# Performance work log

Hardware: AMD Instinct MI355X
Metric: run time of the kernel (lower is better)

## Reference

```python
import jax, jax.numpy as jnp
import numpy as np

GRID = 128
N = GRID * GRID  # number of torus nodes, node id v = x + GRID * y
HID = 64
OUT = 1
BATCH = 64


def _neighbor_idx():
    # Replicates gen_neighbor_lists: sparse matrices are permutation gathers
    # (A x)[v] = x[neighbor(v)] on a periodic grid.
    idx = np.arange(N)
    xc = idx % GRID
    yc = idx // GRID
    up = xc + ((yc + 1) % GRID) * GRID
    down = xc + ((yc - 1) % GRID) * GRID
    left = (xc - 1) % GRID + yc * GRID
    right = (xc + 1) % GRID + yc * GRID
    return np.stack([up, down, left, right], axis=0).astype(np.int32)  # [4, N]

NBR = jnp.asarray(_neighbor_idx())


def setup_inputs() -> dict:
    key = jax.random.key(0)
    ks = jax.random.split(key, 7)
    s4, sh = 1.0 / np.sqrt(4.0), 1.0 / np.sqrt(HID)
    return {
        "x": jax.random.normal(ks[0], (BATCH, N, 2), dtype=jnp.float32),
        "H": jnp.eye(2, dtype=jnp.float32),
        "W_emb": jax.random.uniform(ks[1], (4, HID), jnp.float32, -s4, s4),
        "b_emb": jax.random.uniform(ks[2], (HID,), jnp.float32, -s4, s4),
        "W_hid": jax.random.uniform(ks[3], (HID, HID), jnp.float32, -sh, sh),
        "b_hid": jax.random.uniform(ks[4], (HID,), jnp.float32, -sh, sh),
        "W_post": jax.random.uniform(ks[5], (HID, OUT), jnp.float32, -sh, sh),
        "b_post": jax.random.uniform(ks[6], (OUT,), jnp.float32, -sh, sh),
    }


def reference(x, H, W_emb, b_emb, W_hid, b_hid, W_post, b_post):
    # Permutation-matrix sparse.mm == direct neighbor gather: [B, 4, N, 2]
    xn = x[:, NBR, :]
    # Bilinear form per direction/node: s[b,i,k] = sum_{m,n} x[b,i,m] H[m,n] xn[b,k,i,n]
    s = jnp.einsum('bim,bkin,mn->bik', x, xn, H)  # [B, N, 4]
    h = jax.nn.relu(s @ W_emb + b_emb)            # [B, N, HID]
    h = jax.nn.relu(h @ W_hid + b_hid)            # [B, N, HID]
    h = h @ W_post + b_post                       # [B, N, OUT]
    return h.sum(axis=1)                          # [B, OUT]
```

## Files before the change

kernel.cpp:

```cpp
#include <hip/hip_runtime.h>
#include <hip/hip_bf16.h>

#define GRID_D 128
#define NSITES (GRID_D * GRID_D)
#define HID 64
#define BATCH 64

#define WPB 4
#define BLOCKS 2048
#define BLOCKS_PER_BATCH (BLOCKS / BATCH)
#define WAVES_PER_BATCH (BLOCKS_PER_BATCH * WPB)
#define TILES_PER_WAVE (NSITES / (WAVES_PER_BATCH * 16))

typedef short bf16x8 __attribute__((ext_vector_type(8)));
typedef float f32x4  __attribute__((ext_vector_type(4)));

__device__ __forceinline__ unsigned short f2bf(float f) {
    return __builtin_bit_cast(unsigned short, __float2bfloat16(f));
}

__device__ __forceinline__ unsigned cvt_pk_bf16(float a, float b) {
    unsigned r;
    asm("v_cvt_pk_bf16_f32 %0, %1, %2" : "=v"(r) : "v"(a), "v"(b));
    return r;
}

union frag_u { bf16x8 v; unsigned u[4]; unsigned short us[8]; };

__global__ __launch_bounds__(256)
void gauge_mfma(const float* __restrict__ x,
                const float* __restrict__ H,
                const float* __restrict__ W_emb,
                const float* __restrict__ b_emb,
                const float* __restrict__ W_hid,
                const float* __restrict__ b_hid,
                const float* __restrict__ W_post,
                float* __restrict__ ws)
{
    const int tid   = threadIdx.x;
    const int lane  = tid & 63;
    const int widx  = tid >> 6;
    const int wgid  = blockIdx.x * WPB + widx;
    const int b     = wgid / WAVES_PER_BATCH;
    const int wslot = wgid % WAVES_PER_BATCH;

    const int  ls  = lane & 15;
    const int  kg  = lane >> 4;
    const bool kg0 = (kg == 0);

    const float h00 = H[0], h01 = H[1], h10 = H[2], h11 = H[3];

    bf16x8 bfrag[4][2];
    #pragma unroll
    for (int t = 0; t < 4; ++t) {
        #pragma unroll
        for (int s = 0; s < 2; ++s) {
            frag_u r;
            #pragma unroll
            for (int i = 0; i < 8; ++i) {
                const int khid = s * 32 + ((i & 4) << 2) + (kg << 2) + (i & 3);
                r.us[i] = f2bf(W_hid[khid * HID + t * 16 + ls]);
            }
            bfrag[t][s] = r.v;
        }
    }

    bf16x8 afe[4];
    #pragma unroll
    for (int m = 0; m < 4; ++m) {
        const int col = m * 16 + ls;
        const float w0 = W_emb[0 * HID + col];
        const float w1 = W_emb[1 * HID + col];
        const float w2 = W_emb[2 * HID + col];
        const float w3 = W_emb[3 * HID + col];
        const float bb = b_emb[col];
        frag_u r;
        r.u[0] = kg0 ? cvt_pk_bf16(w0, w1) : 0u;
        r.u[1] = kg0 ? cvt_pk_bf16(w2, w3) : 0u;
        r.u[2] = kg0 ? (unsigned)f2bf(bb) : 0u;
        r.u[3] = 0u;
        afe[m] = r.v;
    }

    float bh[4], wp[4];
    #pragma unroll
    for (int t = 0; t < 4; ++t) {
        bh[t] = b_hid[t * 16 + ls];
        wp[t] = W_post[t * 16 + ls];
    }

    const float* __restrict__ xb = x + (size_t)b * NSITES * 2;
    const int wbase = wslot * (16 * TILES_PER_WAVE);
    const unsigned sd2 = kg0 ? 0x00003F80u : 0u;
    float o = 0.0f;

    for (int tile = 0; tile < TILES_PER_WAVE; ++tile) {
        const int site = wbase + tile * 16 + ls;
        const int xc = site & (GRID_D - 1);
        const int yc = site >> 7;
        const int n0 = xc + (((yc + 1) & (GRID_D - 1)) << 7);
        const int n1 = xc + (((yc - 1) & (GRID_D - 1)) << 7);
        const int n2 = ((xc - 1) & (GRID_D - 1)) + (yc << 7);
        const int n3 = ((xc + 1) & (GRID_D - 1)) + (yc << 7);

        const float2 xi = *(const float2*)(xb + 2 * site);
        const float2 xu = *(const float2*)(xb + 2 * n0);
        const float2 xd = *(const float2*)(xb + 2 * n1);
        const float2 xl = *(const float2*)(xb + 2 * n2);
        const float2 xr = *(const float2*)(xb + 2 * n3);

        const float s0 = xi.x * fmaf(h00, xu.x, h01 * xu.y) + xi.y * fmaf(h10, xu.x, h11 * xu.y);
        const float s1 = xi.x * fmaf(h00, xd.x, h01 * xd.y) + xi.y * fmaf(h10, xd.x, h11 * xd.y);
        const float s2 = xi.x * fmaf(h00, xl.x, h01 * xl.y) + xi.y * fmaf(h10, xl.x, h11 * xl.y);
        const float s3 = xi.x * fmaf(h00, xr.x, h01 * xr.y) + xi.y * fmaf(h10, xr.x, h11 * xr.y);

        frag_u bs;
        const unsigned p01 = cvt_pk_bf16(s0, s1);
        const unsigned p23 = cvt_pk_bf16(s2, s3);
        bs.u[0] = kg0 ? p01 : 0u;
        bs.u[1] = kg0 ? p23 : 0u;
        bs.u[2] = sd2;
        bs.u[3] = 0u;

        f32x4 D0 = {0.f, 0.f, 0.f, 0.f};
        f32x4 D1 = {0.f, 0.f, 0.f, 0.f};
        f32x4 D2 = {0.f, 0.f, 0.f, 0.f};
        f32x4 D3 = {0.f, 0.f, 0.f, 0.f};
        D0 = __builtin_amdgcn_mfma_f32_16x16x32_bf16(afe[0], bs.v, D0, 0, 0, 0);
        D1 = __builtin_amdgcn_mfma_f32_16x16x32_bf16(afe[1], bs.v, D1, 0, 0, 0);
        D2 = __builtin_amdgcn_mfma_f32_16x16x32_bf16(afe[2], bs.v, D2, 0, 0, 0);
        D3 = __builtin_amdgcn_mfma_f32_16x16x32_bf16(afe[3], bs.v, D3, 0, 0, 0);

        #pragma unroll
        for (int r = 0; r < 4; ++r) {
            D0[r] = fmaxf(D0[r], 0.0f);
            D1[r] = fmaxf(D1[r], 0.0f);
            D2[r] = fmaxf(D2[r], 0.0f);
            D3[r] = fmaxf(D3[r], 0.0f);
        }
        frag_u ah0, ah1;
        ah0.u[0] = cvt_pk_bf16(D0[0], D0[1]);
        ah0.u[1] = cvt_pk_bf16(D0[2], D0[3]);
        ah0.u[2] = cvt_pk_bf16(D1[0], D1[1]);
        ah0.u[3] = cvt_pk_bf16(D1[2], D1[3]);
        ah1.u[0] = cvt_pk_bf16(D2[0], D2[1]);
        ah1.u[1] = cvt_pk_bf16(D2[2], D2[3]);
        ah1.u[2] = cvt_pk_bf16(D3[0], D3[1]);
        ah1.u[3] = cvt_pk_bf16(D3[2], D3[3]);

        #pragma unroll
        for (int t = 0; t < 4; ++t) {
            f32x4 acc = { bh[t], bh[t], bh[t], bh[t] };
            acc = __builtin_amdgcn_mfma_f32_16x16x32_bf16(ah0.v, bfrag[t][0], acc, 0, 0, 0);
            acc = __builtin_amdgcn_mfma_f32_16x16x32_bf16(ah1.v, bfrag[t][1], acc, 0, 0, 0);
            #pragma unroll
            for (int r = 0; r < 4; ++r)
                o = fmaf(fmaxf(acc[r], 0.0f), wp[t], o);
        }
    }

    #pragma unroll
    for (int off = 32; off > 0; off >>= 1)
        o += __shfl_down(o, off, 64);

    __shared__ float part[WPB];
    if (lane == 0) part[widx] = o;
    __syncthreads();
    if (tid == 0)
        ws[blockIdx.x] = part[0] + part[1] + part[2] + part[3];
}

__global__ __launch_bounds__(64)
void gauge_reduce(const float* __restrict__ ws,
                  const float* __restrict__ b_post,
                  float* __restrict__ out)
{
    const int b = threadIdx.x;
    float t = (float)NSITES * b_post[0];
    #pragma unroll
    for (int j = 0; j < BLOCKS_PER_BATCH; ++j)
        t += ws[b * BLOCKS_PER_BATCH + j];
    out[b] = t;
}

extern "C" void kernel_launch(void* const* d_in, const int* in_sizes, int n_in,
                              void* d_out, int out_size, void* d_ws, size_t ws_size,
                              hipStream_t stream)
{
    const float* x      = (const float*)d_in[0];
    const float* H      = (const float*)d_in[1];
    const float* W_emb  = (const float*)d_in[2];
    const float* b_emb  = (const float*)d_in[3];
    const float* W_hid  = (const float*)d_in[4];
    const float* b_hid  = (const float*)d_in[5];
    const float* W_post = (const float*)d_in[6];
    const float* b_post = (const float*)d_in[7];
    float* out = (float*)d_out;
    float* ws  = (float*)d_ws;

    gauge_mfma<<<dim3(BLOCKS), dim3(256), 0, stream>>>(
        x, H, W_emb, b_emb, W_hid, b_hid, W_post, ws);
    gauge_reduce<<<dim3(1), dim3(64), 0, stream>>>(ws, b_post, out);
}
```

Before: 97.05 us.

## Compute bilinear features across all 64 lanes and shuffle into MFMA tiles

Before, each tile of 16 sites had all four lane groups load the same five neighbour values and compute the same bilinear features, so the work was done four times over. Now each lane computes features for its own site in a 64-site chunk, and four ds_bpermute shuffles per group supply each 16-site MFMA tile. This removes redundant global loads and VALU math. It also splits the output accumulator into four independent chains, and converts W_hid to bf16 in pairs during setup. The cost is extra cross-lane shuffles and somewhat more register pressure from the larger unrolled body.

Result: no change. 96.88 us (-0.2%).

```diff
diff --git a/kernel.cpp b/kernel.cpp
--- a/kernel.cpp
+++ b/kernel.cpp
@@ -10,7 +10,8 @@
 #define BLOCKS 2048
 #define BLOCKS_PER_BATCH (BLOCKS / BATCH)
 #define WAVES_PER_BATCH (BLOCKS_PER_BATCH * WPB)
-#define TILES_PER_WAVE (NSITES / (WAVES_PER_BATCH * 16))
+#define SITES_PER_WAVE (NSITES / WAVES_PER_BATCH)
+#define ITERS (SITES_PER_WAVE / 64)
 
 typedef short bf16x8 __attribute__((ext_vector_type(8)));
 typedef float f32x4  __attribute__((ext_vector_type(4)));
@@ -57,9 +58,11 @@
         for (int s = 0; s < 2; ++s) {
             frag_u r;
             #pragma unroll
-            for (int i = 0; i < 8; ++i) {
+            for (int j = 0; j < 4; ++j) {
+                const int i    = 2 * j;
                 const int khid = s * 32 + ((i & 4) << 2) + (kg << 2) + (i & 3);
-                r.us[i] = f2bf(W_hid[khid * HID + t * 16 + ls]);
+                r.u[j] = cvt_pk_bf16(W_hid[khid * HID + t * 16 + ls],
+                                     W_hid[(khid + 1) * HID + t * 16 + ls]);
             }
             bfrag[t][s] = r.v;
         }
@@ -69,15 +72,10 @@
     #pragma unroll
     for (int m = 0; m < 4; ++m) {
         const int col = m * 16 + ls;
-        const float w0 = W_emb[0 * HID + col];
-        const float w1 = W_emb[1 * HID + col];
-        const float w2 = W_emb[2 * HID + col];
-        const float w3 = W_emb[3 * HID + col];
-        const float bb = b_emb[col];
         frag_u r;
-        r.u[0] = kg0 ? cvt_pk_bf16(w0, w1) : 0u;
-        r.u[1] = kg0 ? cvt_pk_bf16(w2, w3) : 0u;
-        r.u[2] = kg0 ? (unsigned)f2bf(bb) : 0u;
+        r.u[0] = kg0 ? cvt_pk_bf16(W_emb[0 * HID + col], W_emb[1 * HID + col]) : 0u;
+        r.u[1] = kg0 ? cvt_pk_bf16(W_emb[2 * HID + col], W_emb[3 * HID + col]) : 0u;
+        r.u[2] = kg0 ? (unsigned)f2bf(b_emb[col]) : 0u;
         r.u[3] = 0u;
         afe[m] = r.v;
     }
@@ -90,12 +88,12 @@
     }
 
     const float* __restrict__ xb = x + (size_t)b * NSITES * 2;
-    const int wbase = wslot * (16 * TILES_PER_WAVE);
+    const int wbase = wslot * SITES_PER_WAVE;
     const unsigned sd2 = kg0 ? 0x00003F80u : 0u;
-    float o = 0.0f;
-
-    for (int tile = 0; tile < TILES_PER_WAVE; ++tile) {
-        const int site = wbase + tile * 16 + ls;
+    float o0 = 0.f, o1 = 0.f, o2 = 0.f, o3 = 0.f;
+
+    for (int it = 0; it < ITERS; ++it) {
+        const int site = wbase + it * 64 + lane;
         const int xc = site & (GRID_D - 1);
         const int yc = site >> 7;
         const int n0 = xc + (((yc + 1) & (GRID_D - 1)) << 7);
@@ -114,50 +112,77 @@
         const float s2 = xi.x * fmaf(h00, xl.x, h01 * xl.y) + xi.y * fmaf(h10, xl.x, h11 * xl.y);
         const float s3 = xi.x * fmaf(h00, xr.x, h01 * xr.y) + xi.y * fmaf(h10, xr.x, h11 * xr.y);
 
-        frag_u bs;
         const unsigned p01 = cvt_pk_bf16(s0, s1);
         const unsigned p23 = cvt_pk_bf16(s2, s3);
-        bs.u[0] = kg0 ? p01 : 0u;
-        bs.u[1] = kg0 ? p23 : 0u;
-        bs.u[2] = sd2;
-        bs.u[3] = 0u;
-
-        f32x4 D0 = {0.f, 0.f, 0.f, 0.f};
-        f32x4 D1 = {0.f, 0.f, 0.f, 0.f};
-        f32x4 D2 = {0.f, 0.f, 0.f, 0.f};
-        f32x4 D3 = {0.f, 0.f, 0.f, 0.f};
-        D0 = __builtin_amdgcn_mfma_f32_16x16x32_bf16(afe[0], bs.v, D0, 0, 0, 0);
-        D1 = __builtin_amdgcn_mfma_f32_16x16x32_bf16(afe[1], bs.v, D1, 0, 0, 0);
-        D2 = __builtin_amdgcn_mfma_f32_16x16x32_bf16(afe[2], bs.v, D2, 0, 0, 0);
-        D3 = __builtin_amdgcn_mfma_f32_16x16x32_bf16(afe[3], bs.v, D3, 0, 0, 0);
 
         #pragma unroll
-        for (int r = 0; r < 4; ++r) {
-            D0[r] = fmaxf(D0[r], 0.0f);
-            D1[r] = fmaxf(D1[r], 0.0f);
-            D2[r] = fmaxf(D2[r], 0.0f);
-            D3[r] = fmaxf(D3[r], 0.0f);
+        for (int g = 0; g < 4; ++g) {
+            const unsigned q0 = __shfl(p01, (g << 4) + ls, 64);
+            const unsigned q1 = __shfl(p23, (g << 4) + ls, 64);
+            frag_u bs;
+            bs.u[0] = kg0 ? q0 : 0u;
+            bs.u[1] = kg0 ? q1 : 0u;
+            bs.u[2] = sd2;
+            bs.u[3] = 0u;
+
+            f32x4 D0 = {0.f, 0.f, 0.f, 0.f};
+            f32x4 D1 = {0.f, 0.f, 0.f, 0.f};
+            f32x4 D2 = {0.f, 0.f, 0.f, 0.f};
+            f32x4 D3 = {0.f, 0.f, 0.f, 0.f};
+            D0 = __builtin_amdgcn_mfma_f32_16x16x32_bf16(afe[0], bs.v, D0, 0, 0, 0);
+            D1 = __builtin_amdgcn_mfma_f32_16x16x32_bf16(afe[1], bs.v, D1, 0, 0, 0);
+            D2 = __builtin_amdgcn_mfma_f32_16x16x32_bf16(afe[2], bs.v, D2, 0, 0, 0);
+            D3 = __builtin_amdgcn_mfma_f32_16x16x32_bf16(afe[3], bs.v, D3, 0, 0, 0);
+
+            #pragma unroll
+            for (int r = 0; r < 4; ++r) {
+                D0[r] = fmaxf(D0[r], 0.0f);
+                D1[r] = fmaxf(D1[r], 0.0f);
+                D2[r] = fmaxf(D2[r], 0.0f);
+                D3[r] = fmaxf(D3[r], 0.0f);
+            }
+            frag_u ah0, ah1;
+            ah0.u[0] = cvt_pk_bf16(D0[0], D0[1]);
+            ah0.u[1] = cvt_pk_bf16(D0[2], D0[3]);
+            ah0.u[2] = cvt_pk_bf16(D1[0], D1[1]);
+            ah0.u[3] = cvt_pk_bf16(D1[2], D1[3]);
+            ah1.u[0] = cvt_pk_bf16(D2[0], D2[1]);
+            ah1.u[1] = cvt_pk_bf16(D2[2], D2[3]);
+            ah1.u[2] = cvt_pk_bf16(D3[0], D3[1]);
+            ah1.u[3] = cvt_pk_bf16(D3[2], D3[3]);
+
+            {
+                f32x4 acc = { bh[0], bh[0], bh[0], bh[0] };
+                acc = __builtin_amdgcn_mfma_f32_16x16x32_bf16(ah0.v, bfrag[0][0], acc, 0, 0, 0);
+                acc = __builtin_amdgcn_mfma_f32_16x16x32_bf16(ah1.v, bfrag[0][1], acc, 0, 0, 0);
+                #pragma unroll
+                for (int r = 0; r < 4; ++r) o0 = fmaf(fmaxf(acc[r], 0.0f), wp[0], o0);
+            }
+            {
+                f32x4 acc = { bh[1], bh[1], bh[1], bh[1] };
+                acc = __builtin_amdgcn_mfma_f32_16x16x32_bf16(ah0.v, bfrag[1][0], acc, 0, 0, 0);
+                acc = __builtin_amdgcn_mfma_f32_16x16x32_bf16(ah1.v, bfrag[1][1], acc, 0, 0, 0);
+                #pragma unroll
+                for (int r = 0; r < 4; ++r) o1 = fmaf(fmaxf(acc[r], 0.0f), wp[1], o1);
+            }
+            {
+                f32x4 acc = { bh[2], bh[2], bh[2], bh[2] };
+                acc = __builtin_amdgcn_mfma_f32_16x16x32_bf16(ah0.v, bfrag[2][0], acc, 0, 0, 0);
+                acc = __builtin_amdgcn_mfma_f32_16x16x32_bf16(ah1.v, bfrag[2][1], acc, 0, 0, 0);
+                #pragma unroll
+                for (int r = 0; r < 4; ++r) o2 = fmaf(fmaxf(acc[r], 0.0f), wp[2], o2);
+            }
+            {
+                f32x4 acc = { bh[3], bh[3], bh[3], bh[3] };
+                acc = __builtin_amdgcn_mfma_f32_16x16x32_bf16(ah0.v, bfrag[3][0], acc, 0, 0, 0);
+                acc = __builtin_amdgcn_mfma_f32_16x16x32_bf16(ah1.v, bfrag[3][1], acc, 0, 0, 0);
+                #pragma unroll
+                for (int r = 0; r < 4; ++r) o3 = fmaf(fmaxf(acc[r], 0.0f), wp[3], o3);
+            }
         }
-        frag_u ah0, ah1;
-        ah0.u[0] = cvt_pk_bf16(D0[0], D0[1]);
-        ah0.u[1] = cvt_pk_bf16(D0[2], D0[3]);
-        ah0.u[2] = cvt_pk_bf16(D1[0], D1[1]);
-        ah0.u[3] = cvt_pk_bf16(D1[2], D1[3]);
-        ah1.u[0] = cvt_pk_bf16(D2[0], D2[1]);
-        ah1.u[1] = cvt_pk_bf16(D2[2], D2[3]);
-        ah1.u[2] = cvt_pk_bf16(D3[0], D3[1]);
-        ah1.u[3] = cvt_pk_bf16(D3[2], D3[3]);
-
-        #pragma unroll
-        for (int t = 0; t < 4; ++t) {
-            f32x4 acc = { bh[t], bh[t], bh[t], bh[t] };
-            acc = __builtin_amdgcn_mfma_f32_16x16x32_bf16(ah0.v, bfrag[t][0], acc, 0, 0, 0);
-            acc = __builtin_amdgcn_mfma_f32_16x16x32_bf16(ah1.v, bfrag[t][1], acc, 0, 0, 0);
-            #pragma unroll
-            for (int r = 0; r < 4; ++r)
-                o = fmaf(fmaxf(acc[r], 0.0f), wp[t], o);
-        }
-    }
+    }
+
+    float o = (o0 + o1) + (o2 + o3);
 
     #pragma unroll
     for (int off = 32; off > 0; off >>= 1)
```
